# Kernel optimization log

Hardware: AMD Instinct MI355X
Metric: run time of the kernel (lower is better)

The kernel has to match this reference:

```python
import jax, jax.numpy as jnp
import numpy as np

N, F, H, R, E = 50000, 128, 128, 8, 800000
BN_EPS = 1e-5


def setup_inputs() -> dict:
    key = jax.random.key(0)
    ks = jax.random.split(key, 10)
    g = lambda k, shp: jax.random.normal(k, shp, dtype=jnp.float32) * (1.0 / np.sqrt(shp[-2] if len(shp) > 1 else shp[-1]))
    return {
        "x": jax.random.normal(ks[0], (N, F), dtype=jnp.float32),
        "edge_index": jax.random.randint(ks[1], (2, E), 0, N, dtype=jnp.int32),
        "edge_type": jax.random.randint(ks[2], (E,), 0, R, dtype=jnp.int32),
        "W1": g(ks[3], (F, H)),
        "b1": jnp.zeros((H,), jnp.float32),
        "weight": g(ks[4], (R, H, H)),
        "root": g(ks[5], (H, H)),
        "bias_c": jnp.zeros((H,), jnp.float32),
        "gamma": jnp.ones((H,), jnp.float32),
        "beta": jnp.zeros((H,), jnp.float32),
        "W2": g(ks[6], (H, H)),
        "b2": jnp.zeros((H,), jnp.float32),
        "Wo": g(ks[7], (H, 1)),
        "bo": jnp.zeros((1,), jnp.float32),
    }


def reference(x, edge_index, edge_type, W1, b1, weight, root, bias_c, gamma, beta, W2, b2, Wo, bo):
    n = x.shape[0]
    r = weight.shape[0]
    src, dst = edge_index[0], edge_index[1]
    # segment id combining relation and destination node: equivalent to the
    # per-relation edge-mask + scatter-add loop in RGCNConv, but in one pass.
    seg = edge_type.astype(jnp.int32) * n + dst

    def conv(h):
        msg = h[src]                                            # [E, H] gather
        agg = jax.ops.segment_sum(msg, seg, num_segments=r * n)  # [R*N, H]
        agg = agg.reshape(r, n, -1)                             # [R, N, H]
        out = jnp.einsum('rnc,rco->no', agg, weight)            # per-relation matmul, summed
        return out + h @ root + bias_c

    def bn(h):
        mu = h.mean(axis=0)
        var = h.var(axis=0)  # biased var, matches torch BN training normalization
        return gamma * (h - mu) * jax.lax.rsqrt(var + BN_EPS) + beta

    h = x @ W1 + b1
    h = jax.nn.relu(bn(conv(h)))
    h = jax.nn.relu(bn(conv(h)))
    h = h @ W2 + b2
    h = h @ Wo + bo
    return jax.nn.sigmoid(h)
```

## Files before the change

kernel.cpp:

```cpp
#include <hip/hip_runtime.h>
#include <stdint.h>

typedef __bf16 bf16;
typedef __bf16 bf16x8 __attribute__((ext_vector_type(8)));
typedef float f32x4 __attribute__((ext_vector_type(4)));

__device__ __forceinline__ float bfbits2f(uint32_t lo16) {
    uint32_t b = lo16 << 16;
    float f;
    __builtin_memcpy(&f, &b, 4);
    return f;
}

__device__ __forceinline__ uint32_t pack2bf(float a, float b) {
    uint32_t lo = __builtin_bit_cast(unsigned short, (bf16)a);
    uint32_t hi = __builtin_bit_cast(unsigned short, (bf16)b);
    return lo | (hi << 16);
}

__device__ __forceinline__ void gload_lds16(const void* g, void* l) {
    __builtin_amdgcn_global_load_lds((const __attribute__((address_space(1))) void*)g,
                                     (__attribute__((address_space(3))) void*)l, 16, 0, 0);
}

__global__ void k_prep(const float* __restrict__ W1, const float* __restrict__ weight,
                       const float* __restrict__ root, const float* __restrict__ W2,
                       const float* __restrict__ b2, const float* __restrict__ Wo,
                       const float* __restrict__ bo, bf16* __restrict__ W1T,
                       bf16* __restrict__ WcatT2, float* __restrict__ qc, int R, int ldt) {
    int total = 16384 * (R + 2);
    for (int i = blockIdx.x * blockDim.x + threadIdx.x; i < total + 129; i += gridDim.x * blockDim.x) {
        if (i < 16384) {
            int f = i >> 7, h = i & 127;
            W1T[h * 128 + f] = (bf16)W1[f * 128 + h];
        } else if (i < total) {
            int j = i - 16384;
            int r = j >> 14, rem = j & 16383, c = rem >> 7, o = rem & 127;
            float v = (r < R) ? weight[(size_t)(r * 128 + c) * 128 + o] : root[c * 128 + o];
            WcatT2[(size_t)o * ldt + r * 128 + c] = (bf16)v;
        } else {
            int t = i - total;
            if (t < 128) {
                float s = 0.f;
                for (int j = 0; j < 128; j++) s += W2[t * 128 + j] * Wo[j];
                qc[t] = s;
            } else {
                float c = bo[0];
                for (int j = 0; j < 128; j++) c += b2[j] * Wo[j];
                qc[128] = c;
            }
        }
    }
}

__global__ void k_hist(const int* __restrict__ dst, int* __restrict__ cnt, int E) {
    for (int e = blockIdx.x * blockDim.x + threadIdx.x; e < E; e += gridDim.x * blockDim.x)
        atomicAdd(&cnt[dst[e]], 1);
}

__global__ __launch_bounds__(256) void k_scan_blk(const int* __restrict__ cnt, int* __restrict__ bsum, int N) {
    int i = blockIdx.x * 256 + threadIdx.x;
    int v = (i < N) ? cnt[i] : 0;
#pragma unroll
    for (int d = 1; d < 64; d <<= 1) v += __shfl_xor(v, d);
    __shared__ int ws[4];
    if ((threadIdx.x & 63) == 0) ws[threadIdx.x >> 6] = v;
    __syncthreads();
    if (threadIdx.x == 0) bsum[blockIdx.x] = ws[0] + ws[1] + ws[2] + ws[3];
}

__global__ __launch_bounds__(256) void k_scan_top(int* __restrict__ bsum, int nb) {
    __shared__ int s[256];
    int t = threadIdx.x;
    int v = (t < nb) ? bsum[t] : 0;
    s[t] = v;
    __syncthreads();
#pragma unroll
    for (int d = 1; d < 256; d <<= 1) {
        int u = (t >= d) ? s[t - d] : 0;
        __syncthreads();
        s[t] += u;
        __syncthreads();
    }
    if (t < nb) bsum[t] = s[t] - v;
}

__global__ __launch_bounds__(256) void k_scan_apply(const int* __restrict__ cnt, const int* __restrict__ bsum,
                                                    int* __restrict__ row_off, int* __restrict__ cursor, int N) {
    int b = blockIdx.x, t = threadIdx.x;
    int i = b * 256 + t;
    int v = (i < N) ? cnt[i] : 0;
    int lane = t & 63, wid = t >> 6;
    int incl = v;
#pragma unroll
    for (int d = 1; d < 64; d <<= 1) {
        int u = __shfl_up(incl, d);
        if (lane >= d) incl += u;
    }
    __shared__ int ws[4];
    if (lane == 63) ws[wid] = incl;
    __syncthreads();
    int woff = 0;
    for (int wj = 0; wj < 4; wj++)
        if (wj < wid) woff += ws[wj];
    int excl = bsum[b] + woff + incl - v;
    if (i < N) {
        row_off[i] = excl;
        cursor[i] = excl;
        if (i == N - 1) row_off[N] = excl + v;
    }
}

__global__ void k_fill(const int* __restrict__ src, const int* __restrict__ dst,
                       const int* __restrict__ etype, int* __restrict__ cursor,
                       int* __restrict__ csr, int E, int pbase) {
    int p = blockIdx.x & 7;
    int bg = blockIdx.x >> 3;
    int nchunk = gridDim.x >> 3;
    int chunk = (E + nchunk - 1) / nchunk;
    int beg = bg * chunk, end = min(beg + chunk, E);
    int lo = p * pbase, hi = lo + pbase;
    for (int e = beg + (int)threadIdx.x; e < end; e += blockDim.x) {
        int d = dst[e];
        if (d >= lo && d < hi) {
            int pos = atomicAdd(&cursor[d], 1);
            csr[pos] = (etype[e] << 16) | src[e];
        }
    }
}

__global__ __launch_bounds__(256) void k_gemm0(const float* __restrict__ A, const bf16* __restrict__ BT,
                                               const float* __restrict__ bias, bf16* __restrict__ C, int M) {
    __shared__ bf16 sA[128 * 128];
    __shared__ bf16 sB[128 * 128];
    int tid = threadIdx.x;
    int m0 = blockIdx.x * 128;
#pragma unroll
    for (int i = 0; i < 8; i++) {
        int chunk = i * 256 + tid;
        int row = chunk >> 4, c16 = chunk & 15;
        int sw = ((c16 ^ (row & 7)) << 3);
        int gr = m0 + row;
        int4 va = {0, 0, 0, 0};
        if (gr < M) {
            const float* ap = A + (size_t)gr * 128 + (c16 << 3);
            float4 f0 = *reinterpret_cast<const float4*>(ap);
            float4 f1 = *reinterpret_cast<const float4*>(ap + 4);
            bf16 tmp[8] = {(bf16)f0.x, (bf16)f0.y, (bf16)f0.z, (bf16)f0.w,
                           (bf16)f1.x, (bf16)f1.y, (bf16)f1.z, (bf16)f1.w};
            __builtin_memcpy(&va, tmp, 16);
        }
        *reinterpret_cast<int4*>(&sA[row * 128 + sw]) = va;
        int4 vb = *reinterpret_cast<const int4*>(&BT[(size_t)row * 128 + (c16 << 3)]);
        *reinterpret_cast<int4*>(&sB[row * 128 + sw]) = vb;
    }
    __syncthreads();

    int lane = tid & 63, w = tid >> 6;
    int wm = (w >> 1) * 64, wn = (w & 1) * 64;
    int lr = lane & 15, lk = lane >> 4;
    f32x4 zero = {0.f, 0.f, 0.f, 0.f};
    f32x4 acc[4][4];
#pragma unroll
    for (int mi = 0; mi < 4; mi++)
#pragma unroll
        for (int ni = 0; ni < 4; ni++) acc[mi][ni] = zero;

#pragma unroll
    for (int kk = 0; kk < 4; kk++) {
        int c = (kk << 2) + lk;
        bf16x8 af[4], bfr[4];
#pragma unroll
        for (int mi = 0; mi < 4; mi++) {
            int r = wm + mi * 16 + lr;
            af[mi] = *reinterpret_cast<const bf16x8*>(&sA[r * 128 + ((c ^ (r & 7)) << 3)]);
        }
#pragma unroll
        for (int ni = 0; ni < 4; ni++) {
            int r = wn + ni * 16 + lr;
            bfr[ni] = *reinterpret_cast<const bf16x8*>(&sB[r * 128 + ((c ^ (r & 7)) << 3)]);
        }
#pragma unroll
        for (int mi = 0; mi < 4; mi++)
#pragma unroll
            for (int ni = 0; ni < 4; ni++)
                acc[mi][ni] = __builtin_amdgcn_mfma_f32_16x16x32_bf16(af[mi], bfr[ni], acc[mi][ni], 0, 0, 0);
    }

#pragma unroll
    for (int ni = 0; ni < 4; ni++) {
        int col = wn + ni * 16 + lr;
        float bia = bias[col];
#pragma unroll
        for (int mi = 0; mi < 4; mi++) {
#pragma unroll
            for (int j = 0; j < 4; j++) {
                int row = m0 + wm + mi * 16 + lk * 4 + j;
                if (row < M) C[(size_t)row * 128 + col] = (bf16)(acc[mi][ni][j] + bia);
            }
        }
    }
}

__global__ __launch_bounds__(128) void k_agg2(const bf16* __restrict__ h, const int* __restrict__ row_off,
                                              const int* __restrict__ csr, bf16* __restrict__ G, int N) {
    __shared__ float acc[2][8 * 128];
    int wi = threadIdx.x >> 6;
    int n = blockIdx.x * 2 + wi;
    if (n >= N) return;
    int lane = threadIdx.x & 63;
    int c0 = lane * 2;
    float* a = acc[wi];
#pragma unroll
    for (int i = 0; i < 16; i++) a[i * 64 + lane] = 0.f;
    int beg = row_off[n], end = row_off[n + 1];
    int i = beg;
    for (; i + 4 <= end; i += 4) {
        int p0 = csr[i], p1 = csr[i + 1], p2 = csr[i + 2], p3 = csr[i + 3];
        uint32_t v0 = *reinterpret_cast<const uint32_t*>(&h[(size_t)(p0 & 0xffff) * 128 + c0]);
        uint32_t v1 = *reinterpret_cast<const uint32_t*>(&h[(size_t)(p1 & 0xffff) * 128 + c0]);
        uint32_t v2 = *reinterpret_cast<const uint32_t*>(&h[(size_t)(p2 & 0xffff) * 128 + c0]);
        uint32_t v3 = *reinterpret_cast<const uint32_t*>(&h[(size_t)(p3 & 0xffff) * 128 + c0]);
        float* a0 = &a[(p0 >> 16) * 128 + c0];
        a0[0] += bfbits2f(v0 & 0xffffu); a0[1] += bfbits2f(v0 >> 16);
        float* a1 = &a[(p1 >> 16) * 128 + c0];
        a1[0] += bfbits2f(v1 & 0xffffu); a1[1] += bfbits2f(v1 >> 16);
        float* a2 = &a[(p2 >> 16) * 128 + c0];
        a2[0] += bfbits2f(v2 & 0xffffu); a2[1] += bfbits2f(v2 >> 16);
        float* a3 = &a[(p3 >> 16) * 128 + c0];
        a3[0] += bfbits2f(v3 & 0xffffu); a3[1] += bfbits2f(v3 >> 16);
    }
    for (; i < end; i++) {
        int p = csr[i];
        uint32_t v = *reinterpret_cast<const uint32_t*>(&h[(size_t)(p & 0xffff) * 128 + c0]);
        float* ap = &a[(p >> 16) * 128 + c0];
        ap[0] += bfbits2f(v & 0xffffu);
        ap[1] += bfbits2f(v >> 16);
    }
    size_t gbase = (size_t)n * 1024 + c0;
#pragma unroll
    for (int r = 0; r < 8; r++) {
        __builtin_nontemporal_store(pack2bf(a[r * 128 + c0], a[r * 128 + c0 + 1]),
                                    reinterpret_cast<uint32_t*>(&G[gbase + r * 128]));
    }
}

__global__ __launch_bounds__(256) void k_gemm2(const bf16* __restrict__ G, const bf16* __restrict__ hsrc,
                                               const bf16* __restrict__ BT, const float* __restrict__ bias,
                                               float* __restrict__ C, float* __restrict__ stats,
                                               int M, int K) {
    __shared__ bf16 sA[2][128 * 64];
    __shared__ bf16 sB[2][128 * 64];
    __shared__ float csum[128], csum2[128];
    int tid = threadIdx.x;
    if (tid < 128) { csum[tid] = 0.f; csum2[tid] = 0.f; }
    int m0 = blockIdx.x * 128;
    int lane = tid & 63, w = tid >> 6;
    int wm = (w >> 1) * 64, wn = (w & 1) * 64;
    int lr = lane & 15, lk = lane >> 4;
    int KT = K >> 6;
    int KG = (K - 128) >> 6;
    size_t ldg = (size_t)(K - 128);

    int rowi[4], csi[4], grA[4];
#pragma unroll
    for (int i = 0; i < 4; i++) {
        int chunkid = i * 256 + tid;
        rowi[i] = chunkid >> 3;
        csi[i] = ((chunkid & 7) ^ (rowi[i] & 7)) << 3;
        int g = m0 + rowi[i];
        grA[i] = g < M ? g : M - 1;
    }

    auto stage = [&](int kt, int b) {
        bool lastt = (kt >= KG);
        const bf16* Abase = lastt ? hsrc : G;
        size_t ldA = lastt ? 128 : ldg;
        int ka = lastt ? ((kt - KG) << 6) : (kt << 6);
        int k0 = kt << 6;
        bf16* dA = &sA[b][(w << 6) * 8];
        bf16* dB = &sB[b][(w << 6) * 8];
#pragma unroll
        for (int i = 0; i < 4; i++) {
            gload_lds16(Abase + (size_t)grA[i] * ldA + ka + csi[i], dA + i * 2048);
            gload_lds16(&BT[(size_t)rowi[i] * K + k0 + csi[i]], dB + i * 2048);
        }
    };

    f32x4 zero = {0.f, 0.f, 0.f, 0.f};
    f32x4 acc[4][4];
#pragma unroll
    for (int mi = 0; mi < 4; mi++)
#pragma unroll
        for (int ni = 0; ni < 4; ni++) acc[mi][ni] = zero;

    stage(0, 0);
    stage(1, 1);
    for (int kt = 0; kt < KT; kt++) {
        if (kt + 1 < KT)
            asm volatile("s_waitcnt vmcnt(8)" ::: "memory");
        else
            asm volatile("s_waitcnt vmcnt(0)" ::: "memory");
        __builtin_amdgcn_s_barrier();
        int b = kt & 1;
        const bf16* A = sA[b];
        const bf16* B = sB[b];
#pragma unroll
        for (int kk = 0; kk < 2; kk++) {
            int c = (kk << 2) + lk;
            bf16x8 af[4], bfr[4];
#pragma unroll
            for (int mi = 0; mi < 4; mi++) {
                int r = wm + mi * 16 + lr;
                af[mi] = *reinterpret_cast<const bf16x8*>(&A[r * 64 + ((c ^ (r & 7)) << 3)]);
            }
#pragma unroll
            for (int ni = 0; ni < 4; ni++) {
                int r = wn + ni * 16 + lr;
                bfr[ni] = *reinterpret_cast<const bf16x8*>(&B[r * 64 + ((c ^ (r & 7)) << 3)]);
            }
#pragma unroll
            for (int mi = 0; mi < 4; mi++)
#pragma unroll
                for (int ni = 0; ni < 4; ni++)
                    acc[mi][ni] = __builtin_amdgcn_mfma_f32_16x16x32_bf16(af[mi], bfr[ni], acc[mi][ni], 0, 0, 0);
        }
        __builtin_amdgcn_s_barrier();
        if (kt + 2 < KT) stage(kt + 2, b);
    }

    float ls[4], ls2[4];
#pragma unroll
    for (int ni = 0; ni < 4; ni++) { ls[ni] = 0.f; ls2[ni] = 0.f; }
#pragma unroll
    for (int ni = 0; ni < 4; ni++) {
        int col = wn + ni * 16 + lr;
        float bia = bias[col];
#pragma unroll
        for (int mi = 0; mi < 4; mi++) {
#pragma unroll
            for (int j = 0; j < 4; j++) {
                int row = m0 + wm + mi * 16 + lk * 4 + j;
                if (row < M) {
                    float val = acc[mi][ni][j] + bia;
                    C[(size_t)row * 128 + col] = val;
                    ls[ni] += val;
                    ls2[ni] += val * val;
                }
            }
        }
    }
#pragma unroll
    for (int ni = 0; ni < 4; ni++) {
        float s = ls[ni], s2 = ls2[ni];
        s += __shfl_xor(s, 16); s += __shfl_xor(s, 32);
        s2 += __shfl_xor(s2, 16); s2 += __shfl_xor(s2, 32);
        if (lk == 0) {
            int col = wn + ni * 16 + lr;
            atomicAdd(&csum[col], s);
            atomicAdd(&csum2[col], s2);
        }
    }
    __syncthreads();
    if (tid < 128) {
        atomicAdd(&stats[tid], csum[tid]);
        atomicAdd(&stats[128 + tid], csum2[tid]);
    }
}

__global__ void k_bnfin(float* __restrict__ stats, const float* __restrict__ gamma,
                        const float* __restrict__ beta, float* __restrict__ bnp, float invN) {
    int t = threadIdx.x;
    float mu = stats[t] * invN;
    float var = stats[128 + t] * invN - mu * mu;
    float sc = gamma[t] * rsqrtf(var + 1e-5f);
    bnp[t] = sc;
    bnp[128 + t] = beta[t] - mu * sc;
    stats[t] = 0.f;
    stats[128 + t] = 0.f;
}

__global__ void k_bnrelu(const float* __restrict__ conv, const float* __restrict__ bnp,
                         bf16* __restrict__ h, int N) {
    int total = N * 32;
    for (int i = blockIdx.x * blockDim.x + threadIdx.x; i < total; i += gridDim.x * blockDim.x) {
        int c4 = (i & 31) << 2;
        float4 v = *reinterpret_cast<const float4*>(&conv[(size_t)i * 4]);
        const float* vv = &v.x;
        uint64_t pk = 0;
#pragma unroll
        for (int j = 0; j < 4; j++) {
            int c = c4 + j;
            float val = fmaxf(vv[j] * bnp[c] + bnp[128 + c], 0.f);
            unsigned short us = __builtin_bit_cast(unsigned short, (bf16)val);
            pk |= (uint64_t)us << (16 * j);
        }
        *reinterpret_cast<uint64_t*>(&h[(size_t)i * 4]) = pk;
    }
}

__global__ __launch_bounds__(256) void k_bnout(const float* __restrict__ conv, const float* __restrict__ bnp,
                                               const float* __restrict__ qc, float* __restrict__ out, int N) {
    int wi = threadIdx.x >> 6;
    int n = blockIdx.x * 4 + wi;
    if (n >= N) return;
    int lane = threadIdx.x & 63;
    int c0 = lane * 2;
    float2 v = *reinterpret_cast<const float2*>(&conv[(size_t)n * 128 + c0]);
    float v0 = fmaxf(v.x * bnp[c0] + bnp[128 + c0], 0.f);
    float v1 = fmaxf(v.y * bnp[c0 + 1] + bnp[128 + c0 + 1], 0.f);
    float s = v0 * qc[c0] + v1 * qc[c0 + 1];
#pragma unroll
    for (int d = 1; d < 64; d <<= 1) s += __shfl_xor(s, d);
    if (lane == 0) out[n] = 1.f / (1.f + expf(-(s + qc[128])));
}

extern "C" void kernel_launch(void* const* d_in, const int* in_sizes, int n_in,
                              void* d_out, int out_size, void* d_ws, size_t ws_size,
                              hipStream_t stream) {
    const float* x      = (const float*)d_in[0];
    const int*   ei     = (const int*)d_in[1];
    const int*   etype  = (const int*)d_in[2];
    const float* W1     = (const float*)d_in[3];
    const float* b1     = (const float*)d_in[4];
    const float* weight = (const float*)d_in[5];
    const float* root   = (const float*)d_in[6];
    const float* bias_c = (const float*)d_in[7];
    const float* gamma  = (const float*)d_in[8];
    const float* beta   = (const float*)d_in[9];
    const float* W2     = (const float*)d_in[10];
    const float* b2     = (const float*)d_in[11];
    const float* Wo     = (const float*)d_in[12];
    const float* bo     = (const float*)d_in[13];
    float* out = (float*)d_out;

    int H = in_sizes[4];
    int F = in_sizes[3] / H;
    int N = in_sizes[0] / F;
    int E = in_sizes[2];
    int R = in_sizes[5] / (H * H);
    int ldt = (R + 1) * H;

    const int* srcv = ei;
    const int* dstv = ei + E;

    char* p = (char*)d_ws;
    auto alloc = [&](size_t bytes) -> char* {
        char* r = p;
        p += (bytes + 255) & ~(size_t)255;
        return r;
    };
    bf16*  G       = (bf16*)alloc((size_t)N * (R * H) * 2);
    bf16*  h       = (bf16*)alloc((size_t)N * H * 2);
    float* conv    = (float*)alloc((size_t)N * H * 4);
    bf16*  WcatT2  = (bf16*)alloc((size_t)ldt * H * 2);
    bf16*  W1T     = (bf16*)alloc((size_t)F * H * 2);
    float* qc      = (float*)alloc(129 * 4);
    int*   cnt     = (int*)alloc((size_t)N * 4);
    int*   row_off = (int*)alloc((size_t)(N + 1) * 4);
    int*   cursor  = (int*)alloc((size_t)N * 4);
    int*   csr     = (int*)alloc((size_t)E * 4);
    float* stats   = (float*)alloc(256 * 4);
    float* bnp     = (float*)alloc(256 * 4);
    int*   bsum    = (int*)alloc(256 * 4);
    if ((size_t)(p - (char*)d_ws) > ws_size) return;

    int nb = (N + 255) / 256;
    int pbase = (N + 7) / 8;

    hipMemsetAsync(cnt, 0, (size_t)N * 4, stream);
    hipMemsetAsync(stats, 0, 256 * 4, stream);
    k_prep<<<256, 256, 0, stream>>>(W1, weight, root, W2, b2, Wo, bo, W1T, WcatT2, qc, R, ldt);
    k_hist<<<1024, 256, 0, stream>>>(dstv, cnt, E);
    k_scan_blk<<<nb, 256, 0, stream>>>(cnt, bsum, N);
    k_scan_top<<<1, 256, 0, stream>>>(bsum, nb);
    k_scan_apply<<<nb, 256, 0, stream>>>(cnt, bsum, row_off, cursor, N);
    k_fill<<<1024, 256, 0, stream>>>(srcv, dstv, etype, cursor, csr, E, pbase);

    int mb = (N + 127) / 128;
    k_gemm0<<<mb, 256, 0, stream>>>(x, W1T, b1, h, N);

    for (int l = 0; l < 2; l++) {
        k_agg2<<<(N + 1) / 2, 128, 0, stream>>>(h, row_off, csr, G, N);
        k_gemm2<<<mb, 256, 0, stream>>>(G, h, WcatT2, bias_c, conv, stats, N, ldt);
        k_bnfin<<<1, 128, 0, stream>>>(stats, gamma, beta, bnp, 1.f / (float)N);
        if (l == 0)
            k_bnrelu<<<2048, 256, 0, stream>>>(conv, bnp, h, N);
        else
            k_bnout<<<(N + 3) / 4, 256, 0, stream>>>(conv, bnp, qc, out, N);
    }
}
```

Baseline: 306.4 us.

## Shrink GEMM M-tile to 64 rows and split N across warps

The conv GEMM now uses 64-row blocks instead of 128, with each of the four warps covering all 64 rows and a 32-column slice, which doubles the grid to about 782 blocks and spreads it better across CUs. LDS use for A halves and per-thread accumulators drop from 16 to 8 tiles, which may raise occupancy. BN statistics now go straight to global atomics from each warp, dropping the shared-memory reduction. The cost is that every block reloads the full weight matrix B, so B traffic doubles, and global atomic contention on stats roughly doubles.

```diff
diff --git a/kernel.cpp b/kernel.cpp
--- a/kernel.cpp
+++ b/kernel.cpp
@@ -249,27 +249,31 @@
                                                const bf16* __restrict__ BT, const float* __restrict__ bias,
                                                float* __restrict__ C, float* __restrict__ stats,
                                                int M, int K) {
-    __shared__ bf16 sA[2][128 * 64];
+    __shared__ bf16 sA[2][64 * 64];
     __shared__ bf16 sB[2][128 * 64];
-    __shared__ float csum[128], csum2[128];
     int tid = threadIdx.x;
-    if (tid < 128) { csum[tid] = 0.f; csum2[tid] = 0.f; }
-    int m0 = blockIdx.x * 128;
+    int m0 = blockIdx.x * 64;
     int lane = tid & 63, w = tid >> 6;
-    int wm = (w >> 1) * 64, wn = (w & 1) * 64;
     int lr = lane & 15, lk = lane >> 4;
     int KT = K >> 6;
     int KG = (K - 128) >> 6;
     size_t ldg = (size_t)(K - 128);
 
-    int rowi[4], csi[4], grA[4];
+    int rowA[2], csA[2], grA[2];
+#pragma unroll
+    for (int i = 0; i < 2; i++) {
+        int chunkid = i * 256 + tid;
+        rowA[i] = chunkid >> 3;
+        csA[i] = ((chunkid & 7) ^ (rowA[i] & 7)) << 3;
+        int g = m0 + rowA[i];
+        grA[i] = g < M ? g : M - 1;
+    }
+    int rowB[4], csB[4];
 #pragma unroll
     for (int i = 0; i < 4; i++) {
         int chunkid = i * 256 + tid;
-        rowi[i] = chunkid >> 3;
-        csi[i] = ((chunkid & 7) ^ (rowi[i] & 7)) << 3;
-        int g = m0 + rowi[i];
-        grA[i] = g < M ? g : M - 1;
+        rowB[i] = chunkid >> 3;
+        csB[i] = ((chunkid & 7) ^ (rowB[i] & 7)) << 3;
     }
 
     auto stage = [&](int kt, int b) {
@@ -278,27 +282,28 @@
         size_t ldA = lastt ? 128 : ldg;
         int ka = lastt ? ((kt - KG) << 6) : (kt << 6);
         int k0 = kt << 6;
-        bf16* dA = &sA[b][(w << 6) * 8];
-        bf16* dB = &sB[b][(w << 6) * 8];
-#pragma unroll
-        for (int i = 0; i < 4; i++) {
-            gload_lds16(Abase + (size_t)grA[i] * ldA + ka + csi[i], dA + i * 2048);
-            gload_lds16(&BT[(size_t)rowi[i] * K + k0 + csi[i]], dB + i * 2048);
-        }
+        bf16* dA = &sA[b][w * 512];
+        bf16* dB = &sB[b][w * 512];
+#pragma unroll
+        for (int i = 0; i < 2; i++)
+            gload_lds16(Abase + (size_t)grA[i] * ldA + ka + csA[i], dA + i * 2048);
+#pragma unroll
+        for (int i = 0; i < 4; i++)
+            gload_lds16(&BT[(size_t)rowB[i] * K + k0 + csB[i]], dB + i * 2048);
     };
 
     f32x4 zero = {0.f, 0.f, 0.f, 0.f};
-    f32x4 acc[4][4];
+    f32x4 acc[4][2];
 #pragma unroll
     for (int mi = 0; mi < 4; mi++)
 #pragma unroll
-        for (int ni = 0; ni < 4; ni++) acc[mi][ni] = zero;
+        for (int ni = 0; ni < 2; ni++) acc[mi][ni] = zero;
 
     stage(0, 0);
     stage(1, 1);
     for (int kt = 0; kt < KT; kt++) {
         if (kt + 1 < KT)
-            asm volatile("s_waitcnt vmcnt(8)" ::: "memory");
+            asm volatile("s_waitcnt vmcnt(6)" ::: "memory");
         else
             asm volatile("s_waitcnt vmcnt(0)" ::: "memory");
         __builtin_amdgcn_s_barrier();
@@ -308,63 +313,51 @@
 #pragma unroll
         for (int kk = 0; kk < 2; kk++) {
             int c = (kk << 2) + lk;
-            bf16x8 af[4], bfr[4];
+            bf16x8 af[4], bfr[2];
 #pragma unroll
             for (int mi = 0; mi < 4; mi++) {
-                int r = wm + mi * 16 + lr;
+                int r = mi * 16 + lr;
                 af[mi] = *reinterpret_cast<const bf16x8*>(&A[r * 64 + ((c ^ (r & 7)) << 3)]);
             }
 #pragma unroll
-            for (int ni = 0; ni < 4; ni++) {
-                int r = wn + ni * 16 + lr;
-                bfr[ni] = *reinterpret_cast<const bf16x8*>(&B[r * 64 + ((c ^ (r & 7)) << 3)]);
+            for (int ni = 0; ni < 2; ni++) {
+                int o = (w << 5) + (ni << 4) + lr;
+                bfr[ni] = *reinterpret_cast<const bf16x8*>(&B[o * 64 + ((c ^ (o & 7)) << 3)]);
             }
 #pragma unroll
             for (int mi = 0; mi < 4; mi++)
 #pragma unroll
-                for (int ni = 0; ni < 4; ni++)
+                for (int ni = 0; ni < 2; ni++)
                     acc[mi][ni] = __builtin_amdgcn_mfma_f32_16x16x32_bf16(af[mi], bfr[ni], acc[mi][ni], 0, 0, 0);
         }
         __builtin_amdgcn_s_barrier();
         if (kt + 2 < KT) stage(kt + 2, b);
     }
 
-    float ls[4], ls2[4];
-#pragma unroll
-    for (int ni = 0; ni < 4; ni++) { ls[ni] = 0.f; ls2[ni] = 0.f; }
-#pragma unroll
-    for (int ni = 0; ni < 4; ni++) {
-        int col = wn + ni * 16 + lr;
+#pragma unroll
+    for (int ni = 0; ni < 2; ni++) {
+        int col = (w << 5) + (ni << 4) + lr;
         float bia = bias[col];
+        float s = 0.f, s2 = 0.f;
 #pragma unroll
         for (int mi = 0; mi < 4; mi++) {
 #pragma unroll
             for (int j = 0; j < 4; j++) {
-                int row = m0 + wm + mi * 16 + lk * 4 + j;
+                int row = m0 + mi * 16 + lk * 4 + j;
                 if (row < M) {
                     float val = acc[mi][ni][j] + bia;
                     C[(size_t)row * 128 + col] = val;
-                    ls[ni] += val;
-                    ls2[ni] += val * val;
+                    s += val;
+                    s2 += val * val;
                 }
             }
         }
-    }
-#pragma unroll
-    for (int ni = 0; ni < 4; ni++) {
-        float s = ls[ni], s2 = ls2[ni];
         s += __shfl_xor(s, 16); s += __shfl_xor(s, 32);
         s2 += __shfl_xor(s2, 16); s2 += __shfl_xor(s2, 32);
         if (lk == 0) {
-            int col = wn + ni * 16 + lr;
-            atomicAdd(&csum[col], s);
-            atomicAdd(&csum2[col], s2);
-        }
-    }
-    __syncthreads();
-    if (tid < 128) {
-        atomicAdd(&stats[tid], csum[tid]);
-        atomicAdd(&stats[128 + tid], csum2[tid]);
+            atomicAdd(&stats[col], s);
+            atomicAdd(&stats[128 + col], s2);
+        }
     }
 }
 
@@ -478,11 +471,12 @@
     k_fill<<<1024, 256, 0, stream>>>(srcv, dstv, etype, cursor, csr, E, pbase);
 
     int mb = (N + 127) / 128;
+    int mb64 = (N + 63) / 64;
     k_gemm0<<<mb, 256, 0, stream>>>(x, W1T, b1, h, N);
 
     for (int l = 0; l < 2; l++) {
         k_agg2<<<(N + 1) / 2, 128, 0, stream>>>(h, row_off, csr, G, N);
-        k_gemm2<<<mb, 256, 0, stream>>>(G, h, WcatT2, bias_c, conv, stats, N, ldt);
+        k_gemm2<<<mb64, 256, 0, stream>>>(G, h, WcatT2, bias_c, conv, stats, N, ldt);
         k_bnfin<<<1, 128, 0, stream>>>(stats, gamma, beta, bnp, 1.f / (float)N);
         if (l == 0)
             k_bnrelu<<<2048, 256, 0, stream>>>(conv, bnp, h, N);
```

New measurement: 346.8 us. 13.2% more time.
